# Kernel optimization log

Measured on AMD Instinct MI355X. Metric: run time of the kernel, lower is better.

Reference implementation:

```python
import jax, jax.numpy as jnp
import numpy as np

EMBED_DIM = 1024
NUM_HEADS = 16
HEAD_DIM = EMBED_DIM // NUM_HEADS
L, B, S = 2048, 2, 2048


def setup_inputs() -> dict:
    key = jax.random.key(0)
    k1, k2, k3, k4, k5, k6, k7 = jax.random.split(key, 7)
    query = jax.random.normal(k1, (L, B, EMBED_DIM), dtype=jnp.float32)
    kk = jax.random.normal(k2, (S, B, EMBED_DIM), dtype=jnp.float32)
    vv = jax.random.normal(k3, (S, B, EMBED_DIM), dtype=jnp.float32)
    # in_proj: Linear(E, 3E) -> weight (3E, E), bias (3E,)
    w_in = jax.random.normal(k4, (3 * EMBED_DIM, EMBED_DIM), dtype=jnp.float32) * (1.0 / np.sqrt(EMBED_DIM))
    b_in = jax.random.normal(k5, (3 * EMBED_DIM,), dtype=jnp.float32) * 0.02
    w_out = jax.random.normal(k6, (EMBED_DIM, EMBED_DIM), dtype=jnp.float32) * (1.0 / np.sqrt(EMBED_DIM))
    b_out = jax.random.normal(k7, (EMBED_DIM,), dtype=jnp.float32) * 0.02
    return {"query": query, "key": kk, "value": vv,
            "w_in": w_in, "b_in": b_in, "w_out": w_out, "b_out": b_out}


def _split_heads(x, seq_len, batch):
    # (T, B, E) -> (B, H, T, d)
    return x.reshape(seq_len, batch, NUM_HEADS, HEAD_DIM).transpose(1, 2, 0, 3)


def reference(query, key, value, w_in, b_in, w_out, b_out):
    seq_q, batch, _ = query.shape
    seq_kv = key.shape[0]
    # split fused in_proj into q/k/v projections (chunk along output rows)
    wq, wk, wv = jnp.split(w_in, 3, axis=0)
    bq, bk, bv = jnp.split(b_in, 3, axis=0)
    q = query @ wq.T + bq            # (L, B, E)
    k = key @ wk.T + bk              # (S, B, E)
    v = value @ wv.T + bv            # (S, B, E)
    q = _split_heads(q, seq_q, batch)   # (B, H, L, d)
    k = _split_heads(k, seq_kv, batch)  # (B, H, S, d)
    v = _split_heads(v, seq_kv, batch)  # (B, H, S, d)
    scale = jnp.asarray(np.sqrt(HEAD_DIM), dtype=q.dtype)
    scores = jnp.einsum('bhld,bhsd->bhls', q, k) / scale  # (B, H, L, S)
    attn = jax.nn.softmax(scores, axis=-1)
    context = jnp.einsum('bhls,bhsd->bhld', attn, v)      # (B, H, L, d)
    # (B, H, L, d) -> (L, B, E)
    context = context.transpose(2, 0, 1, 3).reshape(seq_q, batch, EMBED_DIM)
    attn_output = context @ w_out.T + b_out
    return attn_output
```

## Files before the change

kernel.cpp:

```cpp
#include <hip/hip_runtime.h>
#include <hip/hip_bf16.h>
#include <stdint.h>

#define L_SEQ 2048
#define S_SEQ 2048
#define BATCH 2
#define EMB 1024
#define NH 16
#define HD 64
#define MROWS 4096

typedef __bf16 bf16x8 __attribute__((ext_vector_type(8)));
typedef float f32x4 __attribute__((ext_vector_type(4)));
typedef __hip_bfloat16 bf16;

__device__ __forceinline__ f32x4 mfma16(bf16x8 a, bf16x8 b, f32x4 c) {
    return __builtin_amdgcn_mfma_f32_16x16x32_bf16(a, b, c, 0, 0, 0);
}

__device__ __forceinline__ void gll16(const bf16* g, bf16* l) {
    __builtin_amdgcn_global_load_lds(
        (const __attribute__((address_space(1))) void*)g,
        (__attribute__((address_space(3))) void*)l, 16, 0, 0);
}
__device__ __forceinline__ void gllf(const float* g, float* l) {
    __builtin_amdgcn_global_load_lds(
        (const __attribute__((address_space(1))) void*)g,
        (__attribute__((address_space(3))) void*)l, 16, 0, 0);
}

__device__ __forceinline__ bf16x8 ld8_cvt(const float* p) {
    const float4 a = *reinterpret_cast<const float4*>(p);
    const float4 b = *reinterpret_cast<const float4*>(p + 4);
    union { bf16x8 v; bf16 h[8]; } u;
    u.h[0] = __float2bfloat16(a.x); u.h[1] = __float2bfloat16(a.y);
    u.h[2] = __float2bfloat16(a.z); u.h[3] = __float2bfloat16(a.w);
    u.h[4] = __float2bfloat16(b.x); u.h[5] = __float2bfloat16(b.y);
    u.h[6] = __float2bfloat16(b.z); u.h[7] = __float2bfloat16(b.w);
    return u.v;
}

__device__ __forceinline__ uint32_t packbf2(float a, float b) {
    const uint32_t ra = __float_as_uint(a) + 0x8000u;
    const uint32_t rb = __float_as_uint(b) + 0x8000u;
    return __builtin_amdgcn_perm(rb, ra, 0x07060302u);
}

__device__ __forceinline__ bf16x8 pack8(float4 lo, float4 hi) {
    union { uint32_t u[4]; bf16x8 v; } t;
    t.u[0] = packbf2(lo.x, lo.y); t.u[1] = packbf2(lo.z, lo.w);
    t.u[2] = packbf2(hi.x, hi.y); t.u[3] = packbf2(hi.z, hi.w);
    return t.v;
}

__device__ __forceinline__ bf16x8 pfrag(const uint32_t* pk0, const uint32_t* pk1, int sk) {
    auto t0 = __builtin_amdgcn_permlane32_swap(pk0[2 * sk], pk0[2 * sk + 1], false, false);
    auto a02 = __builtin_amdgcn_permlane16_swap(t0[0], t0[1], false, false);
    auto t1 = __builtin_amdgcn_permlane32_swap(pk1[2 * sk], pk1[2 * sk + 1], false, false);
    auto a13 = __builtin_amdgcn_permlane16_swap(t1[0], t1[1], false, false);
    union { uint32_t u[4]; bf16x8 v; } pf;
    pf.u[0] = a02[0]; pf.u[1] = a13[0]; pf.u[2] = a02[1]; pf.u[3] = a13[1];
    return pf.v;
}

__global__ __launch_bounds__(256) void cvt_kernel(
    const float* __restrict__ w_in, const float* __restrict__ w_out,
    bf16* __restrict__ wib, bf16* __restrict__ wob)
{
    const size_t i = ((size_t)blockIdx.x * 256 + threadIdx.x) * 8;
    const size_t o1 = (size_t)3 * EMB * EMB;
    if (i < o1) *reinterpret_cast<bf16x8*>(wib + i) = ld8_cvt(w_in + i);
    else        *reinterpret_cast<bf16x8*>(wob + (i - o1)) = ld8_cvt(w_out + (i - o1));
}

__global__ __launch_bounds__(256) void qkv_gemm(
    const float* __restrict__ Xq, const float* __restrict__ Xk,
    const float* __restrict__ Xv, const bf16* __restrict__ wib,
    const float* __restrict__ b_in,
    bf16* __restrict__ Qh, bf16* __restrict__ Kh, bf16* __restrict__ Vt)
{
    __shared__ alignas(16) float lds_a[2][128 * 32];
    __shared__ alignas(16) bf16  lds_b[2][128 * 32];

    const int tid  = threadIdx.x;
    const int lane = tid & 63;
    const int wv   = tid >> 6;
    const int quad = lane >> 4;
    const int lx   = lane & 15;
    const int lx7  = lane & 7;

    const int m0  = blockIdx.x * 128;
    const int n0g = blockIdx.y * 128;
    const int chunk = n0g >> 10;
    const float* Aop = (chunk == 0) ? Xq : (chunk == 1) ? Xk : Xv;

    const int wm = (wv >> 1) * 64;
    const int wn = (wv & 1) * 64;

    const int arow = tid >> 3;
    const int acs  = ((tid & 7) ^ (arow & 7)) * 4;
    const float* gA = Aop + (size_t)(m0 + arow) * EMB + acs;

    const int gr = 16 * wv + (lane >> 2);
    const int gc = (lane & 3) * 8;
    const bf16* gB = wib + (size_t)(n0g + gr) * EMB + gc;

    f32x4 acc[4][4];
#pragma unroll
    for (int i = 0; i < 4; i++)
#pragma unroll
        for (int j = 0; j < 4; j++) acc[i][j] = (f32x4){0.f, 0.f, 0.f, 0.f};

#pragma unroll
    for (int i = 0; i < 4; i++)
        gllf(gA + (size_t)(i * 32) * EMB, &lds_a[0][i * 1024 + wv * 256]);
    gll16(gB, &lds_b[0][wv * 512]);
    gll16(gB + 64 * EMB, &lds_b[0][wv * 512 + 2048]);
    __syncthreads();

    int cur = 0;
    for (int kt = 0; kt < EMB; kt += 32) {
        if (kt + 32 < EMB) {
            const int nx = cur ^ 1;
#pragma unroll
            for (int i = 0; i < 4; i++)
                gllf(gA + (size_t)(i * 32) * EMB + kt + 32, &lds_a[nx][i * 1024 + wv * 256]);
            gll16(gB + kt + 32, &lds_b[nx][wv * 512]);
            gll16(gB + 64 * EMB + kt + 32, &lds_b[nx][wv * 512 + 2048]);
        }

        bf16x8 af[4], bfv[4];
        const int ka = quad * 8;
        const float* pa = &lds_a[cur][0];
        const bf16*  pb = &lds_b[cur][0];
#pragma unroll
        for (int sm = 0; sm < 4; sm++) {
            const float* pr = pa + (wm + sm * 16 + lx) * 32;
            const float4 lo = *reinterpret_cast<const float4*>(pr + (((2 * quad)     ^ lx7) * 4));
            const float4 hi = *reinterpret_cast<const float4*>(pr + (((2 * quad + 1) ^ lx7) * 4));
            af[sm] = pack8(lo, hi);
        }
#pragma unroll
        for (int sn = 0; sn < 4; sn++)
            bfv[sn] = *reinterpret_cast<const bf16x8*>(pb + (wn + sn * 16 + lx) * 32 + ka);
#pragma unroll
        for (int sm = 0; sm < 4; sm++)
#pragma unroll
            for (int sn = 0; sn < 4; sn++)
                acc[sm][sn] = mfma16(af[sm], bfv[sn], acc[sm][sn]);

        if (kt + 32 < EMB) __syncthreads();
        cur ^= 1;
    }

    const float scale = (chunk == 0) ? 0.18033688011112042f : 1.0f;
    bf16* dst = (chunk == 0) ? Qh : (chunk == 1) ? Kh : Vt;
#pragma unroll
    for (int sn = 0; sn < 4; sn++) {
        const int n_g = n0g + wn + sn * 16 + lx;
        const float bias = b_in[n_g];
        const int nc = n_g & (EMB - 1);
        const int h  = nc >> 6;
        const int dd = nc & 63;
#pragma unroll
        for (int sm = 0; sm < 4; sm++) {
#pragma unroll
            for (int r = 0; r < 4; r++) {
                const int m_g = m0 + wm + sm * 16 + quad * 4 + r;
                const int t = m_g >> 1;
                const int b = m_g & 1;
                const int bhidx = b * NH + h;
                const float v = (acc[sm][sn][r] + bias) * scale;
                const size_t off = (chunk == 2)
                    ? ((size_t)bhidx * HD + dd) * S_SEQ + t
                    : ((size_t)bhidx * S_SEQ + t) * HD + dd;
                dst[off] = __float2bfloat16(v);
            }
        }
    }
}

__global__ __launch_bounds__(256, 2) void attn_kernel(
    const bf16* __restrict__ Qh, const bf16* __restrict__ Kh,
    const bf16* __restrict__ Vt, bf16* __restrict__ ctx)
{
    __shared__ alignas(16) bf16 k_lds[2][128 * 64];
    __shared__ alignas(16) bf16 v_lds[2][64 * 128];

    const int tid  = threadIdx.x;
    const int lane = tid & 63;
    const int wv   = tid >> 6;
    const int quad = lane >> 4;
    const int lx   = lane & 15;
    const int lx7  = lane & 7;

    const int bh = blockIdx.y;
    const int l0 = blockIdx.x * 128;
    const int q0 = wv * 32;

    const bf16* Kbase = Kh + (size_t)bh * S_SEQ * HD;
    const bf16* Vbase = Vt + (size_t)bh * HD * S_SEQ;

    const bf16* qrow = Qh + ((size_t)bh * L_SEQ + l0 + q0 + lx) * HD + quad * 8;
    const bf16x8 qa0 = *reinterpret_cast<const bf16x8*>(qrow);
    const bf16x8 qa1 = *reinterpret_cast<const bf16x8*>(qrow + 32);
    const bf16x8 qb0 = *reinterpret_cast<const bf16x8*>(qrow + 16 * HD);
    const bf16x8 qb1 = *reinterpret_cast<const bf16x8*>(qrow + 16 * HD + 32);

    f32x4 rva = (f32x4){0.f, 0.f, 0.f, 0.f};
    f32x4 rvb = (f32x4){0.f, 0.f, 0.f, 0.f};
    f32x4 acca[4], accb[4];
#pragma unroll
    for (int sn = 0; sn < 4; sn++) {
        acca[sn] = (f32x4){0.f, 0.f, 0.f, 0.f};
        accb[sn] = (f32x4){0.f, 0.f, 0.f, 0.f};
    }

    const int kr = tid >> 3;
    const int kj = tid & 7;
    const bf16* gK = Kbase + (size_t)kr * HD + ((kj ^ (kr & 7)) << 3);
    const int vd = tid >> 4;
    const int vj = tid & 15;
    const bf16* gV = Vbase + (size_t)vd * S_SEQ + ((vj ^ (vd & 7)) << 3);

    bf16* kdst[2] = { &k_lds[0][wv * 512], &k_lds[1][wv * 512] };
    bf16* vdst[2] = { &v_lds[0][wv * 512], &v_lds[1][wv * 512] };

#pragma unroll
    for (int i = 0; i < 4; i++) {
        gll16(gK + (size_t)(i * 32) * HD, kdst[0] + i * 2048);
        gll16(gV + (size_t)(i * 16) * S_SEQ, vdst[0] + i * 2048);
    }

    int cur = 0;
    for (int s0 = 0; s0 < S_SEQ; s0 += 128) {
        __syncthreads();

        if (s0 + 128 < S_SEQ) {
            bf16* kd = kdst[cur ^ 1];
            bf16* vdp = vdst[cur ^ 1];
#pragma unroll
            for (int i = 0; i < 4; i++) {
                gll16(gK + (size_t)(s0 + 128 + i * 32) * HD, kd + i * 2048);
                gll16(gV + (size_t)(i * 16) * S_SEQ + s0 + 128, vdp + i * 2048);
            }
        }
        const bf16* kb = &k_lds[cur][0];
        const bf16* vb = &v_lds[cur][0];

        f32x4 sa[8], sb[8];
#pragma unroll
        for (int c = 0; c < 8; c++) {
            const bf16* krp = kb + (c * 16 + lx) * 64;
            bf16x8 kf0 = *reinterpret_cast<const bf16x8*>(krp + ((quad ^ lx7) << 3));
            bf16x8 kf1 = *reinterpret_cast<const bf16x8*>(krp + (((quad + 4) ^ lx7) << 3));
            f32x4 t0 = (f32x4){0.f, 0.f, 0.f, 0.f};
            t0 = mfma16(kf0, qa0, t0);
            t0 = mfma16(kf1, qa1, t0);
            sa[c] = t0;
            f32x4 t1 = (f32x4){0.f, 0.f, 0.f, 0.f};
            t1 = mfma16(kf0, qb0, t1);
            t1 = mfma16(kf1, qb1, t1);
            sb[c] = t1;
        }

        uint32_t pka0[8], pka1[8], pkb0[8], pkb1[8];
#pragma unroll
        for (int c = 0; c < 8; c++) {
#pragma unroll
            for (int r = 0; r < 4; r++) sa[c][r] = __builtin_amdgcn_exp2f(sa[c][r]);
            rva += sa[c];
            pka0[c] = packbf2(sa[c][0], sa[c][1]);
            pka1[c] = packbf2(sa[c][2], sa[c][3]);
        }
#pragma unroll
        for (int c = 0; c < 8; c++) {
#pragma unroll
            for (int r = 0; r < 4; r++) sb[c][r] = __builtin_amdgcn_exp2f(sb[c][r]);
            rvb += sb[c];
            pkb0[c] = packbf2(sb[c][0], sb[c][1]);
            pkb1[c] = packbf2(sb[c][2], sb[c][3]);
        }

#pragma unroll
        for (int sk = 0; sk < 4; sk++) {
            const bf16x8 pfa = pfrag(pka0, pka1, sk);
            const bf16x8 pfb = pfrag(pkb0, pkb1, sk);
#pragma unroll
            for (int sn = 0; sn < 4; sn++) {
                const bf16x8 vf = *reinterpret_cast<const bf16x8*>(
                    vb + (sn * 16 + lx) * 128 + (((sk * 4 + quad) ^ lx7) << 3));
                acca[sn] = mfma16(pfa, vf, acca[sn]);
                accb[sn] = mfma16(pfb, vf, accb[sn]);
            }
        }
        cur ^= 1;
    }

    float la = (rva[0] + rva[1]) + (rva[2] + rva[3]);
    la += __shfl_xor(la, 16);
    la += __shfl_xor(la, 32);
    float lbs = (rvb[0] + rvb[1]) + (rvb[2] + rvb[3]);
    lbs += __shfl_xor(lbs, 16);
    lbs += __shfl_xor(lbs, 32);

    const int b = bh >> 4;
    const int h = bh & 15;
#pragma unroll
    for (int r = 0; r < 4; r++) {
        const float lra = __shfl(la, quad * 20 + r);
        const float lrb = __shfl(lbs, quad * 20 + r);
        const float inva = 1.f / lra;
        const float invb = 1.f / lrb;
        const int lA = l0 + q0 + quad * 4 + r;
        const int lB = lA + 16;
#pragma unroll
        for (int sn = 0; sn < 4; sn++) {
            const int dd = sn * 16 + lx;
            ctx[(size_t)(lA * BATCH + b) * EMB + h * HD + dd] =
                __float2bfloat16(acca[sn][r] * inva);
            ctx[(size_t)(lB * BATCH + b) * EMB + h * HD + dd] =
                __float2bfloat16(accb[sn][r] * invb);
        }
    }
}

__global__ __launch_bounds__(256) void out_gemm(
    const bf16* __restrict__ ctx, const bf16* __restrict__ wob,
    const float* __restrict__ b_out, float* __restrict__ out)
{
    __shared__ alignas(16) bf16 lds_a[2][64 * 32];
    __shared__ alignas(16) bf16 lds_b[2][128 * 32];

    const int tid  = threadIdx.x;
    const int lane = tid & 63;
    const int wv   = tid >> 6;
    const int quad = lane >> 4;
    const int lx   = lane & 15;

    const int m0 = blockIdx.x * 64;
    const int n0 = blockIdx.y * 128;

    const int wm = (wv >> 1) * 32;
    const int wn = (wv & 1) * 64;

    const int gr = 16 * wv + (lane >> 2);
    const int gc = (lane & 3) * 8;
    const bf16* gA = ctx + (size_t)(m0 + gr) * EMB + gc;
    const bf16* gB = wob + (size_t)(n0 + gr) * EMB + gc;
    bf16* lA = &lds_a[0][wv * 512];
    bf16* lB = &lds_b[0][wv * 512];
    const int BUFA = 64 * 32;
    const int BUFB = 128 * 32;

    f32x4 acc[2][4];
#pragma unroll
    for (int i = 0; i < 2; i++)
#pragma unroll
        for (int j = 0; j < 4; j++) acc[i][j] = (f32x4){0.f, 0.f, 0.f, 0.f};

    gll16(gA, lA);
    gll16(gB, lB);
    gll16(gB + 64 * EMB, lB + 2048);
    __syncthreads();

    int cur = 0;
    for (int kt = 0; kt < EMB; kt += 32) {
        if (kt + 32 < EMB) {
            const int nx = cur ^ 1;
            gll16(gA + kt + 32, lA + nx * BUFA);
            gll16(gB + kt + 32, lB + nx * BUFB);
            gll16(gB + 64 * EMB + kt + 32, lB + nx * BUFB + 2048);
        }

        bf16x8 af[2], bfv[4];
        const int ka = quad * 8;
        const bf16* pa = &lds_a[cur][0];
        const bf16* pb = &lds_b[cur][0];
#pragma unroll
        for (int sm = 0; sm < 2; sm++)
            af[sm] = *reinterpret_cast<const bf16x8*>(pa + (wm + sm * 16 + lx) * 32 + ka);
#pragma unroll
        for (int sn = 0; sn < 4; sn++)
            bfv[sn] = *reinterpret_cast<const bf16x8*>(pb + (wn + sn * 16 + lx) * 32 + ka);
#pragma unroll
        for (int sm = 0; sm < 2; sm++)
#pragma unroll
            for (int sn = 0; sn < 4; sn++)
                acc[sm][sn] = mfma16(af[sm], bfv[sn], acc[sm][sn]);

        if (kt + 32 < EMB) __syncthreads();
        cur ^= 1;
    }

#pragma unroll
    for (int sn = 0; sn < 4; sn++) {
        const int n_g = n0 + wn + sn * 16 + lx;
        const float bias = b_out[n_g];
#pragma unroll
        for (int sm = 0; sm < 2; sm++) {
#pragma unroll
            for (int r = 0; r < 4; r++) {
                const int m_g = m0 + wm + sm * 16 + quad * 4 + r;
                out[(size_t)m_g * EMB + n_g] = acc[sm][sn][r] + bias;
            }
        }
    }
}

extern "C" void kernel_launch(void* const* d_in, const int* in_sizes, int n_in,
                              void* d_out, int out_size, void* d_ws, size_t ws_size,
                              hipStream_t stream)
{
    const float* query = (const float*)d_in[0];
    const float* key_  = (const float*)d_in[1];
    const float* value = (const float*)d_in[2];
    const float* w_in  = (const float*)d_in[3];
    const float* b_in  = (const float*)d_in[4];
    const float* w_out = (const float*)d_in[5];
    const float* b_out = (const float*)d_in[6];
    float* out = (float*)d_out;

    const size_t seg = (size_t)MROWS * EMB;
    bf16* wib = (bf16*)d_ws;
    bf16* wob = wib + (size_t)3 * EMB * EMB;
    bf16* Qh  = wob + (size_t)EMB * EMB;
    bf16* Kh  = Qh + seg;
    bf16* Vt  = Kh + seg;
    bf16* ctx = Vt + seg;

    cvt_kernel<<<2048, 256, 0, stream>>>(w_in, w_out, wib, wob);
    qkv_gemm<<<dim3(32, 24), 256, 0, stream>>>(query, key_, value, wib, b_in, Qh, Kh, Vt);
    attn_kernel<<<dim3(16, 32), 256, 0, stream>>>(Qh, Kh, Vt, ctx);
    out_gemm<<<dim3(64, 8), 256, 0, stream>>>(ctx, wob, b_out, out);
}
```

Baseline: 266.3 us.

## Convert w_in to bf16 inside QKV GEMM via register-staged loads and pack V stores

The separate conversion pass over w_in is dropped. The QKV GEMM now loads both fp32 activations and fp32 weights into registers, converts them to bf16, and writes them to LDS as a software-pipelined prefetch, replacing direct global-to-LDS loads with fp32 A staging. The V epilogue writes pairs of transposed bf16 values as 32-bit stores. The conversion kernel pass and the halved LDS footprint for A are traded for register-staged loads that may expose more latency, and w_in is now converted redundantly by every M-tile block.

```diff
diff --git a/kernel.cpp b/kernel.cpp
--- a/kernel.cpp
+++ b/kernel.cpp
@@ -19,11 +19,6 @@
 }
 
 __device__ __forceinline__ void gll16(const bf16* g, bf16* l) {
-    __builtin_amdgcn_global_load_lds(
-        (const __attribute__((address_space(1))) void*)g,
-        (__attribute__((address_space(3))) void*)l, 16, 0, 0);
-}
-__device__ __forceinline__ void gllf(const float* g, float* l) {
     __builtin_amdgcn_global_load_lds(
         (const __attribute__((address_space(1))) void*)g,
         (__attribute__((address_space(3))) void*)l, 16, 0, 0);
@@ -46,13 +41,6 @@
     return __builtin_amdgcn_perm(rb, ra, 0x07060302u);
 }
 
-__device__ __forceinline__ bf16x8 pack8(float4 lo, float4 hi) {
-    union { uint32_t u[4]; bf16x8 v; } t;
-    t.u[0] = packbf2(lo.x, lo.y); t.u[1] = packbf2(lo.z, lo.w);
-    t.u[2] = packbf2(hi.x, hi.y); t.u[3] = packbf2(hi.z, hi.w);
-    return t.v;
-}
-
 __device__ __forceinline__ bf16x8 pfrag(const uint32_t* pk0, const uint32_t* pk1, int sk) {
     auto t0 = __builtin_amdgcn_permlane32_swap(pk0[2 * sk], pk0[2 * sk + 1], false, false);
     auto a02 = __builtin_amdgcn_permlane16_swap(t0[0], t0[1], false, false);
@@ -64,30 +52,26 @@
 }
 
 __global__ __launch_bounds__(256) void cvt_kernel(
-    const float* __restrict__ w_in, const float* __restrict__ w_out,
-    bf16* __restrict__ wib, bf16* __restrict__ wob)
+    const float* __restrict__ w_out, bf16* __restrict__ wob)
 {
     const size_t i = ((size_t)blockIdx.x * 256 + threadIdx.x) * 8;
-    const size_t o1 = (size_t)3 * EMB * EMB;
-    if (i < o1) *reinterpret_cast<bf16x8*>(wib + i) = ld8_cvt(w_in + i);
-    else        *reinterpret_cast<bf16x8*>(wob + (i - o1)) = ld8_cvt(w_out + (i - o1));
+    *reinterpret_cast<bf16x8*>(wob + i) = ld8_cvt(w_out + i);
 }
 
 __global__ __launch_bounds__(256) void qkv_gemm(
     const float* __restrict__ Xq, const float* __restrict__ Xk,
-    const float* __restrict__ Xv, const bf16* __restrict__ wib,
+    const float* __restrict__ Xv, const float* __restrict__ w_in,
     const float* __restrict__ b_in,
     bf16* __restrict__ Qh, bf16* __restrict__ Kh, bf16* __restrict__ Vt)
 {
-    __shared__ alignas(16) float lds_a[2][128 * 32];
-    __shared__ alignas(16) bf16  lds_b[2][128 * 32];
+    __shared__ alignas(16) bf16 lds_a[2][128 * 32];
+    __shared__ alignas(16) bf16 lds_b[2][128 * 32];
 
     const int tid  = threadIdx.x;
     const int lane = tid & 63;
     const int wv   = tid >> 6;
     const int quad = lane >> 4;
     const int lx   = lane & 15;
-    const int lx7  = lane & 7;
 
     const int m0  = blockIdx.x * 128;
     const int n0g = blockIdx.y * 128;
@@ -97,13 +81,11 @@
     const int wm = (wv >> 1) * 64;
     const int wn = (wv & 1) * 64;
 
-    const int arow = tid >> 3;
-    const int acs  = ((tid & 7) ^ (arow & 7)) * 4;
-    const float* gA = Aop + (size_t)(m0 + arow) * EMB + acs;
-
-    const int gr = 16 * wv + (lane >> 2);
-    const int gc = (lane & 3) * 8;
-    const bf16* gB = wib + (size_t)(n0g + gr) * EMB + gc;
+    const int srow = tid >> 1;
+    const int sc   = (tid & 1) * 16;
+    const float* gA = Aop  + (size_t)(m0  + srow) * EMB + sc;
+    const float* gB = w_in + (size_t)(n0g + srow) * EMB + sc;
+    const int soff = srow * 32 + sc;
 
     f32x4 acc[4][4];
 #pragma unroll
@@ -111,35 +93,47 @@
 #pragma unroll
         for (int j = 0; j < 4; j++) acc[i][j] = (f32x4){0.f, 0.f, 0.f, 0.f};
 
-#pragma unroll
-    for (int i = 0; i < 4; i++)
-        gllf(gA + (size_t)(i * 32) * EMB, &lds_a[0][i * 1024 + wv * 256]);
-    gll16(gB, &lds_b[0][wv * 512]);
-    gll16(gB + 64 * EMB, &lds_b[0][wv * 512 + 2048]);
+    float4 ra[4], rb[4];
+#pragma unroll
+    for (int j = 0; j < 4; j++) {
+        ra[j] = *reinterpret_cast<const float4*>(gA + 4 * j);
+        rb[j] = *reinterpret_cast<const float4*>(gB + 4 * j);
+    }
+    {
+        uint4 ua0, ua1, ub0, ub1;
+        ua0.x = packbf2(ra[0].x, ra[0].y); ua0.y = packbf2(ra[0].z, ra[0].w);
+        ua0.z = packbf2(ra[1].x, ra[1].y); ua0.w = packbf2(ra[1].z, ra[1].w);
+        ua1.x = packbf2(ra[2].x, ra[2].y); ua1.y = packbf2(ra[2].z, ra[2].w);
+        ua1.z = packbf2(ra[3].x, ra[3].y); ua1.w = packbf2(ra[3].z, ra[3].w);
+        ub0.x = packbf2(rb[0].x, rb[0].y); ub0.y = packbf2(rb[0].z, rb[0].w);
+        ub0.z = packbf2(rb[1].x, rb[1].y); ub0.w = packbf2(rb[1].z, rb[1].w);
+        ub1.x = packbf2(rb[2].x, rb[2].y); ub1.y = packbf2(rb[2].z, rb[2].w);
+        ub1.z = packbf2(rb[3].x, rb[3].y); ub1.w = packbf2(rb[3].z, rb[3].w);
+        *reinterpret_cast<uint4*>(&lds_a[0][soff])     = ua0;
+        *reinterpret_cast<uint4*>(&lds_a[0][soff + 8]) = ua1;
+        *reinterpret_cast<uint4*>(&lds_b[0][soff])     = ub0;
+        *reinterpret_cast<uint4*>(&lds_b[0][soff + 8]) = ub1;
+    }
     __syncthreads();
 
     int cur = 0;
     for (int kt = 0; kt < EMB; kt += 32) {
-        if (kt + 32 < EMB) {
-            const int nx = cur ^ 1;
-#pragma unroll
-            for (int i = 0; i < 4; i++)
-                gllf(gA + (size_t)(i * 32) * EMB + kt + 32, &lds_a[nx][i * 1024 + wv * 256]);
-            gll16(gB + kt + 32, &lds_b[nx][wv * 512]);
-            gll16(gB + 64 * EMB + kt + 32, &lds_b[nx][wv * 512 + 2048]);
+        const bool more = (kt + 32 < EMB);
+        if (more) {
+#pragma unroll
+            for (int j = 0; j < 4; j++) {
+                ra[j] = *reinterpret_cast<const float4*>(gA + kt + 32 + 4 * j);
+                rb[j] = *reinterpret_cast<const float4*>(gB + kt + 32 + 4 * j);
+            }
         }
 
         bf16x8 af[4], bfv[4];
         const int ka = quad * 8;
-        const float* pa = &lds_a[cur][0];
-        const bf16*  pb = &lds_b[cur][0];
-#pragma unroll
-        for (int sm = 0; sm < 4; sm++) {
-            const float* pr = pa + (wm + sm * 16 + lx) * 32;
-            const float4 lo = *reinterpret_cast<const float4*>(pr + (((2 * quad)     ^ lx7) * 4));
-            const float4 hi = *reinterpret_cast<const float4*>(pr + (((2 * quad + 1) ^ lx7) * 4));
-            af[sm] = pack8(lo, hi);
-        }
+        const bf16* pa = &lds_a[cur][0];
+        const bf16* pb = &lds_b[cur][0];
+#pragma unroll
+        for (int sm = 0; sm < 4; sm++)
+            af[sm] = *reinterpret_cast<const bf16x8*>(pa + (wm + sm * 16 + lx) * 32 + ka);
 #pragma unroll
         for (int sn = 0; sn < 4; sn++)
             bfv[sn] = *reinterpret_cast<const bf16x8*>(pb + (wn + sn * 16 + lx) * 32 + ka);
@@ -149,32 +143,69 @@
             for (int sn = 0; sn < 4; sn++)
                 acc[sm][sn] = mfma16(af[sm], bfv[sn], acc[sm][sn]);
 
-        if (kt + 32 < EMB) __syncthreads();
+        if (more) {
+            const int nx = cur ^ 1;
+            uint4 ua0, ua1, ub0, ub1;
+            ua0.x = packbf2(ra[0].x, ra[0].y); ua0.y = packbf2(ra[0].z, ra[0].w);
+            ua0.z = packbf2(ra[1].x, ra[1].y); ua0.w = packbf2(ra[1].z, ra[1].w);
+            ua1.x = packbf2(ra[2].x, ra[2].y); ua1.y = packbf2(ra[2].z, ra[2].w);
+            ua1.z = packbf2(ra[3].x, ra[3].y); ua1.w = packbf2(ra[3].z, ra[3].w);
+            ub0.x = packbf2(rb[0].x, rb[0].y); ub0.y = packbf2(rb[0].z, rb[0].w);
+            ub0.z = packbf2(rb[1].x, rb[1].y); ub0.w = packbf2(rb[1].z, rb[1].w);
+            ub1.x = packbf2(rb[2].x, rb[2].y); ub1.y = packbf2(rb[2].z, rb[2].w);
+            ub1.z = packbf2(rb[3].x, rb[3].y); ub1.w = packbf2(rb[3].z, rb[3].w);
+            *reinterpret_cast<uint4*>(&lds_a[nx][soff])     = ua0;
+            *reinterpret_cast<uint4*>(&lds_a[nx][soff + 8]) = ua1;
+            *reinterpret_cast<uint4*>(&lds_b[nx][soff])     = ub0;
+            *reinterpret_cast<uint4*>(&lds_b[nx][soff + 8]) = ub1;
+            __syncthreads();
+        }
         cur ^= 1;
     }
 
     const float scale = (chunk == 0) ? 0.18033688011112042f : 1.0f;
-    bf16* dst = (chunk == 0) ? Qh : (chunk == 1) ? Kh : Vt;
-#pragma unroll
-    for (int sn = 0; sn < 4; sn++) {
-        const int n_g = n0g + wn + sn * 16 + lx;
-        const float bias = b_in[n_g];
-        const int nc = n_g & (EMB - 1);
-        const int h  = nc >> 6;
-        const int dd = nc & 63;
-#pragma unroll
-        for (int sm = 0; sm < 4; sm++) {
-#pragma unroll
-            for (int r = 0; r < 4; r++) {
-                const int m_g = m0 + wm + sm * 16 + quad * 4 + r;
-                const int t = m_g >> 1;
-                const int b = m_g & 1;
-                const int bhidx = b * NH + h;
-                const float v = (acc[sm][sn][r] + bias) * scale;
-                const size_t off = (chunk == 2)
-                    ? ((size_t)bhidx * HD + dd) * S_SEQ + t
-                    : ((size_t)bhidx * S_SEQ + t) * HD + dd;
-                dst[off] = __float2bfloat16(v);
+    if (chunk == 2) {
+#pragma unroll
+        for (int sn = 0; sn < 4; sn++) {
+            const int n_g = n0g + wn + sn * 16 + lx;
+            const float bias = b_in[n_g];
+            const int nc = n_g & (EMB - 1);
+            const int h  = nc >> 6;
+            const int dd = nc & 63;
+            bf16* row0 = Vt + ((size_t)(h * HD + dd)) * S_SEQ;
+            bf16* row1 = Vt + ((size_t)((NH + h) * HD + dd)) * S_SEQ;
+#pragma unroll
+            for (int sm = 0; sm < 4; sm++) {
+                const int mb = m0 + wm + sm * 16 + quad * 4;
+                const int t0 = mb >> 1;
+                const float v0 = acc[sm][sn][0] + bias;
+                const float v1 = acc[sm][sn][1] + bias;
+                const float v2 = acc[sm][sn][2] + bias;
+                const float v3 = acc[sm][sn][3] + bias;
+                *reinterpret_cast<uint32_t*>(row0 + t0) = packbf2(v0, v2);
+                *reinterpret_cast<uint32_t*>(row1 + t0) = packbf2(v1, v3);
+            }
+        }
+    } else {
+        bf16* dst = (chunk == 0) ? Qh : Kh;
+#pragma unroll
+        for (int sn = 0; sn < 4; sn++) {
+            const int n_g = n0g + wn + sn * 16 + lx;
+            const float bias = b_in[n_g];
+            const int nc = n_g & (EMB - 1);
+            const int h  = nc >> 6;
+            const int dd = nc & 63;
+#pragma unroll
+            for (int sm = 0; sm < 4; sm++) {
+#pragma unroll
+                for (int r = 0; r < 4; r++) {
+                    const int m_g = m0 + wm + sm * 16 + quad * 4 + r;
+                    const int t = m_g >> 1;
+                    const int b = m_g & 1;
+                    const int bhidx = b * NH + h;
+                    const float v = (acc[sm][sn][r] + bias) * scale;
+                    dst[((size_t)bhidx * S_SEQ + t) * HD + dd] = __float2bfloat16(v);
+                }
             }
         }
     }
@@ -422,15 +453,14 @@
     float* out = (float*)d_out;
 
     const size_t seg = (size_t)MROWS * EMB;
-    bf16* wib = (bf16*)d_ws;
-    bf16* wob = wib + (size_t)3 * EMB * EMB;
+    bf16* wob = (bf16*)d_ws;
     bf16* Qh  = wob + (size_t)EMB * EMB;
     bf16* Kh  = Qh + seg;
     bf16* Vt  = Kh + seg;
     bf16* ctx = Vt + seg;
 
-    cvt_kernel<<<2048, 256, 0, stream>>>(w_in, w_out, wib, wob);
-    qkv_gemm<<<dim3(32, 24), 256, 0, stream>>>(query, key_, value, wib, b_in, Qh, Kh, Vt);
+    cvt_kernel<<<512, 256, 0, stream>>>(w_out, wob);
+    qkv_gemm<<<dim3(32, 24), 256, 0, stream>>>(query, key_, value, w_in, b_in, Qh, Kh, Vt);
     attn_kernel<<<dim3(16, 32), 256, 0, stream>>>(Qh, Kh, Vt, ctx);
     out_gemm<<<dim3(64, 8), 256, 0, stream>>>(ctx, wob, b_out, out);
 }
```

Result: faster. 258.9 us (-2.8%).
